# Optimization experiments

Measured on AMD Instinct MI355X. Metric: run time of the kernel, lower is better.

The kernel has to match this reference:

```python
import jax, jax.numpy as jnp
import numpy as np

N_USERS = 100000
N_ITEMS = 50000
N_NODES = N_USERS + N_ITEMS
NNZ = 1500000
BATCH = 1048576
DIM = 64
LAYERS = 2


def setup_inputs() -> dict:
    key = jax.random.key(0)
    ks = jax.random.split(key, 10)
    u_idx = jax.random.randint(ks[0], (BATCH,), 0, N_USERS)
    i_idx = jax.random.randint(ks[1], (BATCH,), 0, N_ITEMS)
    A_rows = jax.random.randint(ks[2], (NNZ,), 0, N_NODES)
    A_cols = jax.random.randint(ks[3], (NNZ,), 0, N_NODES)
    A_vals = jax.random.uniform(ks[4], (NNZ,), dtype=jnp.float32)
    Eu = jax.random.normal(ks[5], (N_USERS, DIM), dtype=jnp.float32) * 0.01
    Ei = jax.random.normal(ks[6], (N_ITEMS, DIM), dtype=jnp.float32) * 0.01
    bu = jax.random.normal(ks[7], (N_USERS,), dtype=jnp.float32) * 0.01
    bi = jax.random.normal(ks[8], (N_ITEMS,), dtype=jnp.float32) * 0.01
    mu = jnp.zeros((1,), dtype=jnp.float32)
    return {"u_idx": u_idx, "i_idx": i_idx, "A_rows": A_rows, "A_cols": A_cols,
            "A_vals": A_vals, "Eu": Eu, "Ei": Ei, "bu": bu, "bi": bi, "mu": mu}


def _spmm(vals, rows, cols, H):
    # sparse A (COO) @ H : gather source rows, scale, scatter-add to dest rows
    return jax.ops.segment_sum(vals[:, None] * H[cols], rows, num_segments=N_NODES)


def reference(u_idx, i_idx, A_rows, A_cols, A_vals, Eu, Ei, bu, bi, mu):
    X0 = jnp.concatenate([Eu, Ei], axis=0)  # [N_NODES, DIM]
    H = X0
    for _ in range(LAYERS):
        H = _spmm(A_vals, A_rows, A_cols, H)  # dropout=0 -> identity
    U = H[:N_USERS]
    I = H[N_USERS:]
    pred = jnp.sum(U[u_idx] * I[i_idx], axis=-1)
    pred = pred + bu[u_idx] + bi[i_idx] + mu[0]
    return pred
```

## Files before the change

kernel.cpp:

```cpp
#include <hip/hip_runtime.h>

#define N_USERS 100000
#define N_ITEMS 50000
#define N_NODES 150000
#define NNZ 1500000
#define BATCH 1048576
#define DIM 64

#define BIN_SHIFT 7
#define BIN_ROWS 128
#define NBINS ((N_NODES + BIN_ROWS - 1) / BIN_ROWS)
#define NROWS_PAD (NBINS * BIN_ROWS)
#define CAPB 1536
#define CAPR 15
#define CAPE 8
#define P1_THREADS 512
#define EPT 8
#define EPB (P1_THREADS * EPT)
#define P1_BLOCKS ((NNZ + EPB - 1) / EPB)
#define G_MAX 16384
#define RARE_MAX 4096

typedef unsigned short ushortT;

__device__ __forceinline__ float bf2f(ushortT x) {
    return __uint_as_float(((unsigned)x) << 16);
}
__device__ __forceinline__ ushortT f2bf(float x) {
    unsigned u = __float_as_uint(x);
    return (ushortT)((u + 0x7FFFu + ((u >> 16) & 1u)) >> 16);
}
__device__ __forceinline__ unsigned pack2(float a, float b) {
    unsigned ua = __float_as_uint(a), ub = __float_as_uint(b);
    ua = (ua + 0x7FFFu + ((ua >> 16) & 1u)) >> 16;
    ub = (ub + 0x7FFFu + ((ub >> 16) & 1u)) >> 16;
    return ua | (ub << 16);
}

__global__ void zero_ws(float4* __restrict__ p, int n4) {
    int i = blockIdx.x * blockDim.x + threadIdx.x;
    if (i < n4) p[i] = make_float4(0.f, 0.f, 0.f, 0.f);
}

__global__ void conv_E(const float4* __restrict__ Eu, const float4* __restrict__ Ei,
                       uint2* __restrict__ Eb,
                       int* __restrict__ bin_cursor, int* __restrict__ g_cnt,
                       int* __restrict__ rare_cnt) {
    if (blockIdx.x == 0) {
        for (int i = threadIdx.x; i < NBINS; i += 256) bin_cursor[i] = 0;
        if (threadIdx.x == 0) { *g_cnt = 0; *rare_cnt = 0; }
    }
    int i = blockIdx.x * blockDim.x + threadIdx.x;
    if (i >= (N_USERS + N_ITEMS) * DIM / 4) return;
    float4 x = (i < N_USERS * DIM / 4) ? Eu[i] : Ei[i - N_USERS * DIM / 4];
    Eb[i] = make_uint2(pack2(x.x, x.y), pack2(x.z, x.w));
}

__global__ __launch_bounds__(P1_THREADS)
void p1_bin(const int* __restrict__ rows,
            const int* __restrict__ cols,
            const float* __restrict__ vals,
            int* __restrict__ bin_cursor,
            int2* __restrict__ binned,
            int* __restrict__ g_cnt,
            int4* __restrict__ G,
            int* __restrict__ rare_cnt,
            int* __restrict__ rare) {
    __shared__ int h[NBINS];
    __shared__ int lcnt[NBINS];
    __shared__ int lbase[NBINS + 1];
    __shared__ int2 stage[EPB];
    __shared__ ushortT sbin[EPB];
    int tid = threadIdx.x;
    for (int i = tid; i < NBINS; i += P1_THREADS) lcnt[i] = 0;
    __syncthreads();

    int base_e = blockIdx.x * EPB;
    int re[EPT]; int ce[EPT]; float ve[EPT];
#pragma unroll
    for (int k = 0; k < EPT; ++k) {
        int e = base_e + k * P1_THREADS + tid;
        if (e < NNZ) {
            re[k] = rows[e]; ce[k] = cols[e]; ve[k] = vals[e];
            atomicAdd(&lcnt[re[k] >> BIN_SHIFT], 1);
        } else {
            re[k] = -1; ce[k] = 0; ve[k] = 0.f;
        }
    }
    __syncthreads();

    if (tid < 64) {
        int carry = 0;
        for (int b0 = 0; b0 < NBINS; b0 += 64) {
            int idx = b0 + tid;
            int x = (idx < NBINS) ? lcnt[idx] : 0;
            int incl = x;
#pragma unroll
            for (int off = 1; off < 64; off <<= 1) {
                int t = __shfl_up(incl, off);
                if (tid >= off) incl += t;
            }
            if (idx < NBINS) lbase[idx] = carry + incl - x;
            carry += __shfl(incl, 63);
        }
        if (tid == 0) lbase[NBINS] = carry;
    }
    __syncthreads();

    for (int i = tid; i < NBINS; i += P1_THREADS) {
        int c = lcnt[i];
        h[i] = (c > 0) ? atomicAdd(&bin_cursor[i], c) : 0;
        lcnt[i] = 0;
    }
    __syncthreads();

#pragma unroll
    for (int k = 0; k < EPT; ++k) {
        if (re[k] >= 0) {
            int b = re[k] >> BIN_SHIFT;
            int pos = lbase[b] + atomicAdd(&lcnt[b], 1);
            stage[pos] = make_int2((ce[k] << BIN_SHIFT) | (re[k] & (BIN_ROWS - 1)),
                                   __float_as_int(ve[k]));
            sbin[pos] = (ushortT)b;
        }
    }
    __syncthreads();

    int total = lbase[NBINS];
    for (int j = tid; j < total; j += P1_THREADS) {
        int b = sbin[j];
        int2 cv = stage[j];
        int off = h[b] + (j - lbase[b]);
        if (off < CAPB) {
            binned[(size_t)b * CAPB + off] = cv;
        } else {
            int r = b * BIN_ROWS + (cv.x & (BIN_ROWS - 1));
            int c = (int)(((unsigned)cv.x) >> BIN_SHIFT);
            int p = atomicAdd(g_cnt, 1);
            if (p < G_MAX) G[p] = make_int4(r, c, cv.y, 0);
            int q = atomicAdd(rare_cnt, 1);
            if (q < RARE_MAX) rare[q] = r;
        }
    }
}

__global__ __launch_bounds__(256)
void p2_fill(const int* __restrict__ bin_cursor,
             const int2* __restrict__ binned,
             int* __restrict__ buckets,
             int2* __restrict__ ext,
             int* __restrict__ rare_cnt,
             int* __restrict__ rare) {
    __shared__ int  cnt_s[BIN_ROWS];
    __shared__ int2 rowbuf[BIN_ROWS * CAPR];
    int bin = blockIdx.x, tid = threadIdx.x;
    for (int i = tid; i < BIN_ROWS; i += 256) cnt_s[i] = 0;
    __syncthreads();
    int n = bin_cursor[bin]; if (n > CAPB) n = CAPB;
    for (int i = tid; i < n; i += 256) {
        int2 cv = binned[(size_t)bin * CAPB + i];
        int r = cv.x & (BIN_ROWS - 1);
        int c = (int)(((unsigned)cv.x) >> BIN_SHIFT);
        int slot = atomicAdd(&cnt_s[r], 1);
        if (slot < CAPR) {
            rowbuf[r * CAPR + slot] = make_int2(c, cv.y);
        } else if (slot < CAPR + CAPE) {
            ext[(size_t)(bin * BIN_ROWS + r) * CAPE + (slot - CAPR)] = make_int2(c, cv.y);
        }
    }
    __syncthreads();
    for (int r = tid; r < BIN_ROWS; r += 256) {
        if (cnt_s[r] > CAPR + CAPE) {
            int q = atomicAdd(rare_cnt, 1);
            if (q < RARE_MAX) rare[q] = bin * BIN_ROWS + r;
        }
    }
    int4* dst = (int4*)(buckets + (size_t)bin * BIN_ROWS * 32);
    for (int idx = tid; idx < BIN_ROWS * 8; idx += 256) {
        int r = idx >> 3, q = idx & 7;
        int4 o;
        if (q == 0) {
            int2 t = rowbuf[r * CAPR];
            o = make_int4(cnt_s[r], 0, t.x, t.y);
        } else {
            int2 a = rowbuf[r * CAPR + 2 * q - 1];
            int2 b = rowbuf[r * CAPR + 2 * q];
            o = make_int4(a.x, a.y, b.x, b.y);
        }
        dst[idx] = o;
    }
}

__global__ void spmm_gather16(const int* __restrict__ buckets,
                              const int2* __restrict__ ext,
                              const ushortT* __restrict__ F,
                              ushortT* __restrict__ out) {
    int wv   = (blockIdx.x * blockDim.x + threadIdx.x) >> 6;
    int lane = threadIdx.x & 63;
    int l15  = lane & 15;
    int gb   = lane & 48;
    int r0   = wv << 2;
    if (r0 >= N_NODES) return;
    int row  = r0 + (lane >> 4);

    int2 md = ((const int2*)(buckets + (size_t)r0 * 32))[lane];

    int cnt = __shfl(md.x, gb);
    int nb  = (cnt < CAPR) ? cnt : CAPR;
    int net = cnt - CAPR;
    int ne  = (net < 0) ? 0 : ((net > CAPE) ? CAPE : net);

    uint2 f[CAPR];
#pragma unroll
    for (int k = 0; k < CAPR; ++k) {
        int cs = __shfl(md.x, gb + k + 1);
        int c  = (k < nb) ? cs : 0;
        f[k] = *(const uint2*)(F + ((size_t)c << 6) + (l15 << 2));
    }
    float4 acc = make_float4(0.f, 0.f, 0.f, 0.f);
#pragma unroll
    for (int k = 0; k < CAPR; ++k) {
        int vi = __shfl(md.y, gb + k + 1);
        float v = (k < nb) ? __int_as_float(vi) : 0.f;
        acc.x = fmaf(v, __uint_as_float(f[k].x << 16), acc.x);
        acc.y = fmaf(v, __uint_as_float(f[k].x & 0xFFFF0000u), acc.y);
        acc.z = fmaf(v, __uint_as_float(f[k].y << 16), acc.z);
        acc.w = fmaf(v, __uint_as_float(f[k].y & 0xFFFF0000u), acc.w);
    }

    if (__ballot(ne > 0)) {
        int2 ev = ext[((size_t)row << 3) + (l15 & 7)];
#pragma unroll
        for (int k = 0; k < CAPE; ++k) {
            int cs = __shfl(ev.x, gb + k);
            int vi = __shfl(ev.y, gb + k);
            int c  = (k < ne) ? cs : 0;
            float v = (k < ne) ? __int_as_float(vi) : 0.f;
            uint2 fw = *(const uint2*)(F + ((size_t)c << 6) + (l15 << 2));
            acc.x = fmaf(v, __uint_as_float(fw.x << 16), acc.x);
            acc.y = fmaf(v, __uint_as_float(fw.x & 0xFFFF0000u), acc.y);
            acc.z = fmaf(v, __uint_as_float(fw.y << 16), acc.z);
            acc.w = fmaf(v, __uint_as_float(fw.y & 0xFFFF0000u), acc.w);
        }
    }

    *(uint2*)(out + ((size_t)row << 6) + (l15 << 2)) =
        make_uint2(pack2(acc.x, acc.y), pack2(acc.z, acc.w));
}

__global__ void rare_fix(const int* __restrict__ rare_cnt,
                         const int* __restrict__ rare,
                         const int* __restrict__ bin_cursor,
                         const int2* __restrict__ binned,
                         const int* __restrict__ g_cnt,
                         const int4* __restrict__ G,
                         const ushortT* __restrict__ F,
                         ushortT* __restrict__ out) {
    int lane = threadIdx.x & 63;
    int wv = (blockIdx.x * blockDim.x + threadIdx.x) >> 6;
    int nw = (gridDim.x * blockDim.x) >> 6;
    int n = *rare_cnt; if (n > RARE_MAX) n = RARE_MAX;
    for (int i = wv; i < n; i += nw) {
        int row = rare[i];
        int bin = row >> BIN_SHIFT, rloc = row & (BIN_ROWS - 1);
        int m = bin_cursor[bin]; if (m > CAPB) m = CAPB;
        size_t bb = (size_t)bin * CAPB;
        float acc = 0.f;
        for (int base = 0; base < m; base += 64) {
            int j = base + lane;
            int2 e = (j < m) ? binned[bb + j] : make_int2(0, 0);
            bool match = (j < m) && ((e.x & (BIN_ROWS - 1)) == rloc);
            unsigned long long mask = __ballot(match);
            while (mask) {
                int src = __ffsll(mask) - 1; mask &= mask - 1;
                int c = (int)(((unsigned)__shfl(e.x, src)) >> BIN_SHIFT);
                float v = __int_as_float(__shfl(e.y, src));
                acc = fmaf(v, bf2f(F[((size_t)c << 6) + lane]), acc);
            }
        }
        int gc = *g_cnt; if (gc > G_MAX) gc = G_MAX;
        for (int j = 0; j < gc; ++j) {
            int4 t = G[j];
            if (t.x == row)
                acc = fmaf(__int_as_float(t.z), bf2f(F[((size_t)t.y << 6) + lane]), acc);
        }
        out[((size_t)row << 6) + lane] = f2bf(acc);
    }
}

__global__ void pred_bf16(const int* __restrict__ u_idx,
                          const int* __restrict__ i_idx,
                          const ushortT* __restrict__ F,
                          const float* __restrict__ bu,
                          const float* __restrict__ bi,
                          const float* __restrict__ mu,
                          float* __restrict__ out) {
    int gid = blockIdx.x * blockDim.x + threadIdx.x;
    int t = gid >> 4;
    int s = gid & 15;
    if (t >= BATCH / 2) return;
    int b0 = t, b1 = t + BATCH / 2;
    int u0 = u_idx[b0], i0 = i_idx[b0];
    int u1 = u_idx[b1], i1 = i_idx[b1];
    ushort4 a0 = *((const ushort4*)(F + ((size_t)u0 << 6)) + s);
    ushort4 c0 = *((const ushort4*)(F + ((size_t)(N_USERS + i0) << 6)) + s);
    ushort4 a1 = *((const ushort4*)(F + ((size_t)u1 << 6)) + s);
    ushort4 c1 = *((const ushort4*)(F + ((size_t)(N_USERS + i1) << 6)) + s);
    float p0 = bf2f(a0.x) * bf2f(c0.x) + bf2f(a0.y) * bf2f(c0.y)
             + bf2f(a0.z) * bf2f(c0.z) + bf2f(a0.w) * bf2f(c0.w);
    float p1 = bf2f(a1.x) * bf2f(c1.x) + bf2f(a1.y) * bf2f(c1.y)
             + bf2f(a1.z) * bf2f(c1.z) + bf2f(a1.w) * bf2f(c1.w);
    p0 += __shfl_xor(p0, 1); p1 += __shfl_xor(p1, 1);
    p0 += __shfl_xor(p0, 2); p1 += __shfl_xor(p1, 2);
    p0 += __shfl_xor(p0, 4); p1 += __shfl_xor(p1, 4);
    p0 += __shfl_xor(p0, 8); p1 += __shfl_xor(p1, 8);
    if (s == 0) {
        out[b0] = p0 + bu[u0] + bi[i0] + mu[0];
        out[b1] = p1 + bu[u1] + bi[i1] + mu[0];
    }
}

__global__ void spmm_scatter(const int* __restrict__ rows,
                             const int* __restrict__ cols,
                             const float* __restrict__ vals,
                             const float* __restrict__ Hu,
                             const float* __restrict__ Hi,
                             float* __restrict__ out) {
    int gid = blockIdx.x * blockDim.x + threadIdx.x;
    int e = gid >> 4;
    int s = gid & 15;
    if (e >= NNZ) return;
    int r = rows[e];
    int c = cols[e];
    float v = vals[e];
    const float* src = (c < N_USERS) ? (Hu + (size_t)c * DIM)
                                     : (Hi + (size_t)(c - N_USERS) * DIM);
    float4 x = *reinterpret_cast<const float4*>(src + s * 4);
    float* dst = out + (size_t)r * DIM + s * 4;
    atomicAdd(dst + 0, v * x.x);
    atomicAdd(dst + 1, v * x.y);
    atomicAdd(dst + 2, v * x.z);
    atomicAdd(dst + 3, v * x.w);
}

__global__ void pred_f32(const int* __restrict__ u_idx,
                         const int* __restrict__ i_idx,
                         const float* __restrict__ U,
                         const float* __restrict__ I,
                         const float* __restrict__ bu,
                         const float* __restrict__ bi,
                         const float* __restrict__ mu,
                         float* __restrict__ out) {
    int gid = blockIdx.x * blockDim.x + threadIdx.x;
    int b = gid >> 4;
    int s = gid & 15;
    if (b >= BATCH) return;
    int u = u_idx[b];
    int it = i_idx[b];
    float4 a = *reinterpret_cast<const float4*>(U + (size_t)u * DIM + s * 4);
    float4 c = *reinterpret_cast<const float4*>(I + (size_t)it * DIM + s * 4);
    float p = a.x * c.x + a.y * c.y + a.z * c.z + a.w * c.w;
    p += __shfl_xor(p, 1);
    p += __shfl_xor(p, 2);
    p += __shfl_xor(p, 4);
    p += __shfl_xor(p, 8);
    if (s == 0) out[b] = p + bu[u] + bi[it] + mu[0];
}

extern "C" void kernel_launch(void* const* d_in, const int* in_sizes, int n_in,
                              void* d_out, int out_size, void* d_ws, size_t ws_size,
                              hipStream_t stream) {
    const int*   u_idx  = (const int*)d_in[0];
    const int*   i_idx  = (const int*)d_in[1];
    const int*   A_rows = (const int*)d_in[2];
    const int*   A_cols = (const int*)d_in[3];
    const float* A_vals = (const float*)d_in[4];
    const float* Eu     = (const float*)d_in[5];
    const float* Ei     = (const float*)d_in[6];
    const float* bu     = (const float*)d_in[7];
    const float* bi     = (const float*)d_in[8];
    const float* mu     = (const float*)d_in[9];
    float* out = (float*)d_out;

    char* ws = (char*)d_ws;
    ushortT* H1b       = (ushortT*)(ws);
    ushortT* EbH2b     = (ushortT*)(ws + 19200000);
    int*     buckets   = (int*)    (ws + 38400000);
    int2*    binned    = (int2*)   (ws + 57602048);
    int2*    ext       = (int2*)   (ws + 72003584);
    int*     bin_cursor= (int*)    (ws + 81604608);
    int*     g_cnt     = (int*)    (ws + 81609472);
    int*     rare_cnt  = (int*)    (ws + 81609504);
    int4*    G         = (int4*)   (ws + 81609536);
    int*     rare      = (int*)    (ws + 81871680);
    const size_t NEEDED = 81888064;

    const int pred_blocks   = ((BATCH / 2) * 16 + 255) / 256;
    const int gather_blocks = (N_NODES / 4) * 64 / 256;
    const int conv_blocks   = ((N_USERS + N_ITEMS) * DIM / 4 + 255) / 256;

    if (ws_size >= NEEDED) {
        conv_E<<<conv_blocks, 256, 0, stream>>>((const float4*)Eu, (const float4*)Ei,
                                                (uint2*)EbH2b, bin_cursor, g_cnt, rare_cnt);
        p1_bin<<<P1_BLOCKS, P1_THREADS, 0, stream>>>(A_rows, A_cols, A_vals,
                                                     bin_cursor, binned, g_cnt, G,
                                                     rare_cnt, rare);
        p2_fill<<<NBINS, 256, 0, stream>>>(bin_cursor, binned, buckets, ext, rare_cnt, rare);

        spmm_gather16<<<gather_blocks, 256, 0, stream>>>(buckets, ext, EbH2b, H1b);
        rare_fix<<<32, 256, 0, stream>>>(rare_cnt, rare, bin_cursor, binned, g_cnt, G,
                                         EbH2b, H1b);
        spmm_gather16<<<gather_blocks, 256, 0, stream>>>(buckets, ext, H1b, EbH2b);
        rare_fix<<<32, 256, 0, stream>>>(rare_cnt, rare, bin_cursor, binned, g_cnt, G,
                                         H1b, EbH2b);

        pred_bf16<<<pred_blocks, 256, 0, stream>>>(u_idx, i_idx, EbH2b, bu, bi, mu, out);
    } else {
        float* H1 = (float*)d_ws;
        float* H2 = H1 + (size_t)N_NODES * DIM;
        const int n4 = 2 * N_NODES * DIM / 4;
        zero_ws<<<(n4 + 255) / 256, 256, 0, stream>>>((float4*)d_ws, n4);
        const int spmm_blocks = (NNZ * 16 + 255) / 256;
        spmm_scatter<<<spmm_blocks, 256, 0, stream>>>(A_rows, A_cols, A_vals, Eu, Ei, H1);
        spmm_scatter<<<spmm_blocks, 256, 0, stream>>>(A_rows, A_cols, A_vals,
                                                      H1, H1 + (size_t)N_USERS * DIM, H2);
        const int pf_blocks = (BATCH * 16 + 255) / 256;
        pred_f32<<<pf_blocks, 256, 0, stream>>>(u_idx, i_idx,
                                                H2, H2 + (size_t)N_USERS * DIM,
                                                bu, bi, mu, out);
    }
}
```

Measured before the change: 176.4 us.

## Fuse embedding bf16 conversion with COO binning pass in one interleaved launch

The fp32-to-bf16 embedding conversion and the first edge-binning pass now run as a single kernel, with every eighth block doing binning and the rest doing conversion, so the two independent phases overlap on the GPU. Counter zeroing moves into a tiny separate kernel, which is needed because binning can no longer rely on the conversion kernel having reset the cursors first. Binning blocks grow to 1024 threads with 4 edges each, and the p2 fill uses 512 threads. The cost is an extra launch and large shared memory declared for every block, including conversion blocks that never use it, which may limit occupancy.

```diff
diff --git a/kernel.cpp b/kernel.cpp
--- a/kernel.cpp
+++ b/kernel.cpp
@@ -14,10 +14,13 @@
 #define CAPB 1536
 #define CAPR 15
 #define CAPE 8
-#define P1_THREADS 512
-#define EPT 8
+#define P1_THREADS 1024
+#define EPT 4
 #define EPB (P1_THREADS * EPT)
 #define P1_BLOCKS ((NNZ + EPB - 1) / EPB)
+#define CONV_N ((N_USERS + N_ITEMS) * DIM / 4)
+#define CONV_BLOCKS ((CONV_N + 1023) / 1024)
+#define FUSED_BLOCKS 2944
 #define G_MAX 16384
 #define RARE_MAX 4096
 
@@ -42,40 +45,46 @@
     if (i < n4) p[i] = make_float4(0.f, 0.f, 0.f, 0.f);
 }
 
-__global__ void conv_E(const float4* __restrict__ Eu, const float4* __restrict__ Ei,
-                       uint2* __restrict__ Eb,
-                       int* __restrict__ bin_cursor, int* __restrict__ g_cnt,
-                       int* __restrict__ rare_cnt) {
-    if (blockIdx.x == 0) {
-        for (int i = threadIdx.x; i < NBINS; i += 256) bin_cursor[i] = 0;
-        if (threadIdx.x == 0) { *g_cnt = 0; *rare_cnt = 0; }
-    }
-    int i = blockIdx.x * blockDim.x + threadIdx.x;
-    if (i >= (N_USERS + N_ITEMS) * DIM / 4) return;
-    float4 x = (i < N_USERS * DIM / 4) ? Eu[i] : Ei[i - N_USERS * DIM / 4];
-    Eb[i] = make_uint2(pack2(x.x, x.y), pack2(x.z, x.w));
+__global__ void zero_ctrl(int* __restrict__ bin_cursor, int* __restrict__ g_cnt,
+                          int* __restrict__ rare_cnt) {
+    int i = threadIdx.x;
+    for (int b = i; b < NBINS; b += 1024) bin_cursor[b] = 0;
+    if (i == 0) { *g_cnt = 0; *rare_cnt = 0; }
 }
 
 __global__ __launch_bounds__(P1_THREADS)
-void p1_bin(const int* __restrict__ rows,
-            const int* __restrict__ cols,
-            const float* __restrict__ vals,
-            int* __restrict__ bin_cursor,
-            int2* __restrict__ binned,
-            int* __restrict__ g_cnt,
-            int4* __restrict__ G,
-            int* __restrict__ rare_cnt,
-            int* __restrict__ rare) {
+void fused_conv_p1(const float4* __restrict__ Eu, const float4* __restrict__ Ei,
+                   uint2* __restrict__ Eb,
+                   const int* __restrict__ rows,
+                   const int* __restrict__ cols,
+                   const float* __restrict__ vals,
+                   int* __restrict__ bin_cursor,
+                   int2* __restrict__ binned,
+                   int* __restrict__ g_cnt,
+                   int4* __restrict__ G,
+                   int* __restrict__ rare_cnt,
+                   int* __restrict__ rare) {
+    int tid = threadIdx.x;
+    if ((blockIdx.x & 7) != 7) {
+        int cb = blockIdx.x - (blockIdx.x >> 3);
+        int i = cb * 1024 + tid;
+        if (i < CONV_N) {
+            float4 x = (i < N_USERS * DIM / 4) ? Eu[i] : Ei[i - N_USERS * DIM / 4];
+            Eb[i] = make_uint2(pack2(x.x, x.y), pack2(x.z, x.w));
+        }
+        return;
+    }
+    int pb = blockIdx.x >> 3;
+    if (pb >= P1_BLOCKS) return;
     __shared__ int h[NBINS];
     __shared__ int lcnt[NBINS];
     __shared__ int lbase[NBINS + 1];
     __shared__ int2 stage[EPB];
     __shared__ ushortT sbin[EPB];
-    int tid = threadIdx.x;
     for (int i = tid; i < NBINS; i += P1_THREADS) lcnt[i] = 0;
     __syncthreads();
 
-    int base_e = blockIdx.x * EPB;
+    int base_e = pb * EPB;
     int re[EPT]; int ce[EPT]; float ve[EPT];
 #pragma unroll
     for (int k = 0; k < EPT; ++k) {
@@ -144,7 +153,7 @@
     }
 }
 
-__global__ __launch_bounds__(256)
+__global__ __launch_bounds__(512)
 void p2_fill(const int* __restrict__ bin_cursor,
              const int2* __restrict__ binned,
              int* __restrict__ buckets,
@@ -154,10 +163,10 @@
     __shared__ int  cnt_s[BIN_ROWS];
     __shared__ int2 rowbuf[BIN_ROWS * CAPR];
     int bin = blockIdx.x, tid = threadIdx.x;
-    for (int i = tid; i < BIN_ROWS; i += 256) cnt_s[i] = 0;
+    for (int i = tid; i < BIN_ROWS; i += 512) cnt_s[i] = 0;
     __syncthreads();
     int n = bin_cursor[bin]; if (n > CAPB) n = CAPB;
-    for (int i = tid; i < n; i += 256) {
+    for (int i = tid; i < n; i += 512) {
         int2 cv = binned[(size_t)bin * CAPB + i];
         int r = cv.x & (BIN_ROWS - 1);
         int c = (int)(((unsigned)cv.x) >> BIN_SHIFT);
@@ -169,14 +178,14 @@
         }
     }
     __syncthreads();
-    for (int r = tid; r < BIN_ROWS; r += 256) {
+    for (int r = tid; r < BIN_ROWS; r += 512) {
         if (cnt_s[r] > CAPR + CAPE) {
             int q = atomicAdd(rare_cnt, 1);
             if (q < RARE_MAX) rare[q] = bin * BIN_ROWS + r;
         }
     }
     int4* dst = (int4*)(buckets + (size_t)bin * BIN_ROWS * 32);
-    for (int idx = tid; idx < BIN_ROWS * 8; idx += 256) {
+    for (int idx = tid; idx < BIN_ROWS * 8; idx += 512) {
         int r = idx >> 3, q = idx & 7;
         int4 o;
         if (q == 0) {
@@ -397,15 +406,13 @@
 
     const int pred_blocks   = ((BATCH / 2) * 16 + 255) / 256;
     const int gather_blocks = (N_NODES / 4) * 64 / 256;
-    const int conv_blocks   = ((N_USERS + N_ITEMS) * DIM / 4 + 255) / 256;
 
     if (ws_size >= NEEDED) {
-        conv_E<<<conv_blocks, 256, 0, stream>>>((const float4*)Eu, (const float4*)Ei,
-                                                (uint2*)EbH2b, bin_cursor, g_cnt, rare_cnt);
-        p1_bin<<<P1_BLOCKS, P1_THREADS, 0, stream>>>(A_rows, A_cols, A_vals,
-                                                     bin_cursor, binned, g_cnt, G,
-                                                     rare_cnt, rare);
-        p2_fill<<<NBINS, 256, 0, stream>>>(bin_cursor, binned, buckets, ext, rare_cnt, rare);
+        zero_ctrl<<<1, 1024, 0, stream>>>(bin_cursor, g_cnt, rare_cnt);
+        fused_conv_p1<<<FUSED_BLOCKS, P1_THREADS, 0, stream>>>(
+            (const float4*)Eu, (const float4*)Ei, (uint2*)EbH2b,
+            A_rows, A_cols, A_vals, bin_cursor, binned, g_cnt, G, rare_cnt, rare);
+        p2_fill<<<NBINS, 512, 0, stream>>>(bin_cursor, binned, buckets, ext, rare_cnt, rare);
 
         spmm_gather16<<<gather_blocks, 256, 0, stream>>>(buckets, ext, EbH2b, H1b);
         rare_fix<<<32, 256, 0, stream>>>(rare_cnt, rare, bin_cursor, binned, g_cnt, G,
```

Result: slower. 210.3 us (+19.2%).
